# Optimization experiments

Measured on AMD Instinct MI355X. Metric: run time of the kernel, lower is better.

The kernel has to match this reference:

```python
import jax, jax.numpy as jnp
import numpy as np

N, R, E, DIN, DOUT, B = 40000, 16, 50000, 256, 256, 4


def setup_inputs() -> dict:
    key = jax.random.key(0)
    ks = jax.random.split(key, 7)
    xav = (2.0 / (DIN + DOUT)) ** 0.5  # xavier-ish scale
    x = jax.random.normal(ks[0], (N, DIN), jnp.float32)
    bases = jax.random.normal(ks[1], (B, DIN, DOUT), jnp.float32) * xav
    coeff = jax.random.normal(ks[2], (R, B), jnp.float32) * 0.5
    loop_weight = jax.random.normal(ks[3], (DIN, DOUT), jnp.float32) * xav
    h_bias = jnp.zeros((DOUT,), jnp.float32)
    edge_src = jax.random.randint(ks[4], (R, E), 0, N, dtype=jnp.int64)
    edge_dst = jax.random.randint(ks[5], (R, E), 0, N, dtype=jnp.int64)
    return {"x": x, "bases": bases, "coeff": coeff, "loop_weight": loop_weight,
            "h_bias": h_bias, "edge_src": edge_src, "edge_dst": edge_dst}


def reference(x, bases, coeff, loop_weight, h_bias, edge_src, edge_dst):
    # Basis decomposition: per-relation weight W_r = sum_b coeff[r,b] * bases[b]
    W = jnp.einsum('rb,bio->rio', coeff, bases)  # [R, DIN, DOUT]
    n = x.shape[0]

    def body(acc, rel):
        W_r, src, dst = rel
        # transform all nodes once, gather at edge sources
        m = (x @ W_r)[src]                                   # [E, DOUT]
        agg = jax.ops.segment_sum(m, dst, num_segments=n)    # [N, DOUT]
        deg = jax.ops.segment_sum(jnp.ones(src.shape, jnp.float32), dst,
                                  num_segments=n)            # in-degree per rel
        # norm='right': divide by dst in-degree (clamped to 1)
        return acc + agg / jnp.clip(deg, 1.0)[:, None], None

    h0 = jnp.zeros((n, loop_weight.shape[1]), x.dtype)
    h, _ = jax.lax.scan(body, h0, (W, edge_src, edge_dst))   # sum over relations
    h = h + x @ loop_weight + h_bias                         # self-loop + bias
    return jax.nn.relu(h)
```

## Files before the change

kernel.cpp:

```cpp
#include <hip/hip_runtime.h>

#define NN   40000
#define RR   16
#define EE   50000
#define DD   256
#define NB   4
#define KTOT (NB*DD + DD)
#define BM   64
#define BN   128
#define BK   32

#define SCAN_BLK  40
#define SCAN_ELEM 1024

typedef __bf16 bf16x8 __attribute__((ext_vector_type(8)));
typedef float  f32x4  __attribute__((ext_vector_type(4)));
typedef float  f32x2  __attribute__((ext_vector_type(2)));
typedef unsigned short ushort_t;

__device__ inline unsigned short f2bf(float f) {
    unsigned int b = __builtin_bit_cast(unsigned int, f);
    b += 0x7FFFu + ((b >> 16) & 1u);
    return (unsigned short)(b >> 16);
}


__global__ __launch_bounds__(256) void k_cast(const float* __restrict__ x,
                                              const float* __restrict__ bases,
                                              const float* __restrict__ lw,
                                              ushort_t* __restrict__ xb,
                                              ushort_t* __restrict__ Bt) {
    int t = blockIdx.x * blockDim.x + threadIdx.x;
    const int NX = NN * DD / 4;
    if (t < NX) {
        float4 f = *(const float4*)(x + (size_t)t * 4);
        ushort4 o;
        o.x = f2bf(f.x); o.y = f2bf(f.y); o.z = f2bf(f.z); o.w = f2bf(f.w);
        *(ushort4*)(xb + (size_t)t * 4) = o;
    } else {
        int u = t - NX;
        if (u < DD * KTOT) {
            int o = u / KTOT, k = u - o * KTOT;
            float f = (k < NB * DD) ? bases[(size_t)k * DD + o]
                                    : lw[(size_t)(k - NB * DD) * DD + o];
            Bt[u] = f2bf(f);
        }
    }
}

__global__ __launch_bounds__(256) void k_deg(const int* __restrict__ edst,
                                             int* __restrict__ deg) {
    int e = blockIdx.x * blockDim.x + threadIdx.x;
    if (e >= RR * EE) return;
    int r = e / EE;
    atomicAdd(&deg[r * NN + edst[e]], 1);
}

__global__ __launch_bounds__(256) void k_scanA(const int* __restrict__ deg,
                                               int* __restrict__ offsets,
                                               int* __restrict__ bsum) {
    __shared__ int part[256];
    int t = threadIdx.x, b = blockIdx.x;
    int g = b * SCAN_ELEM + t * 4;
    int4 h = {0, 0, 0, 0};
    if (g < NN) {
#pragma unroll
        for (int r = 0; r < RR; r++) {
            int4 d = *(const int4*)(deg + (size_t)r * NN + g);
            h.x += d.x; h.y += d.y; h.z += d.z; h.w += d.w;
        }
    }
    int s = h.x + h.y + h.z + h.w;
    part[t] = s;
    __syncthreads();
    for (int off = 1; off < 256; off <<= 1) {
        int v = (t >= off) ? part[t - off] : 0;
        __syncthreads();
        part[t] += v;
        __syncthreads();
    }
    int ex = part[t] - s;
    if (g < NN) {
        int4 o;
        o.x = ex;
        o.y = ex + h.x;
        o.z = ex + h.x + h.y;
        o.w = ex + h.x + h.y + h.z;
        *(int4*)(offsets + g) = o;
    }
    if (t == 255) bsum[b] = part[255];
}

__global__ __launch_bounds__(256) void k_scanB(const int* __restrict__ bsum,
                                               int* __restrict__ offsets,
                                               int* __restrict__ cursor) {
    __shared__ int sbase, stot;
    int t = threadIdx.x, b = blockIdx.x;
    if (t == 0) {
        int acc = 0, base = 0;
        for (int i = 0; i < SCAN_BLK; i++) {
            if (i == b) base = acc;
            acc += bsum[i];
        }
        sbase = base;
        stot = acc;
    }
    __syncthreads();
    int base = sbase;
    int g = b * SCAN_ELEM + t * 4;
    if (g < NN) {
        int4 o = *(const int4*)(offsets + g);
        o.x += base; o.y += base; o.z += base; o.w += base;
        *(int4*)(offsets + g) = o;
        *(int4*)(cursor + g) = o;
    }
    if (b == SCAN_BLK - 1 && t == 0) offsets[NN] = stot;
}

__global__ __launch_bounds__(256) void k_escatter(const int* __restrict__ esrc,
                                                  const int* __restrict__ edst,
                                                  int* __restrict__ cursor,
                                                  unsigned int* __restrict__ recs) {
    int e = blockIdx.x * blockDim.x + threadIdx.x;
    if (e >= RR * EE) return;
    int r = e / EE;
    int d = edst[e];
    int pos = atomicAdd(&cursor[d], 1);
    recs[pos] = (unsigned int)esrc[e] | ((unsigned int)r << 16);
}

__global__ __launch_bounds__(256) void k_gather(const ushort_t* __restrict__ xb,
                                                const float* __restrict__ coeff,
                                                const int* __restrict__ deg,
                                                const int* __restrict__ offsets,
                                                const unsigned int* __restrict__ recs,
                                                ushort_t* __restrict__ vb) {
    __shared__ float wtab[4][64];
    int lane = threadIdx.x & 63;
    int wv   = threadIdx.x >> 6;
    int n    = __builtin_amdgcn_readfirstlane(blockIdx.x * 4 + wv);

    {
        int r  = lane >> 2;
        int dg = deg[r * NN + n];
        float inv = 1.0f / (float)(dg > 0 ? dg : 1);
        wtab[wv][lane] = coeff[lane] * inv;
    }

    int beg = offsets[n], end = offsets[n + 1];
    f32x2 a[4][2];
#pragma unroll
    for (int b = 0; b < 4; b++) { a[b][0] = (f32x2){0,0}; a[b][1] = (f32x2){0,0}; }

    const float* wrow = &wtab[wv][0];
    const ushort_t* xl = xb + lane * 4;

    auto acc_edge = [&](uint2 u, float4 w) {
        f32x2 lo, hi;
        lo.x = __builtin_bit_cast(float, u.x << 16);
        lo.y = __builtin_bit_cast(float, u.x & 0xFFFF0000u);
        hi.x = __builtin_bit_cast(float, u.y << 16);
        hi.y = __builtin_bit_cast(float, u.y & 0xFFFF0000u);
        a[0][0] = lo * (f32x2){w.x, w.x} + a[0][0];
        a[0][1] = hi * (f32x2){w.x, w.x} + a[0][1];
        a[1][0] = lo * (f32x2){w.y, w.y} + a[1][0];
        a[1][1] = hi * (f32x2){w.y, w.y} + a[1][1];
        a[2][0] = lo * (f32x2){w.z, w.z} + a[2][0];
        a[2][1] = hi * (f32x2){w.z, w.z} + a[2][1];
        a[3][0] = lo * (f32x2){w.w, w.w} + a[3][0];
        a[3][1] = hi * (f32x2){w.w, w.w} + a[3][1];
    };

    int ei = beg;
    for (; ei + 4 <= end; ei += 4) {
        unsigned int r0 = recs[ei + 0];
        unsigned int r1 = recs[ei + 1];
        unsigned int r2 = recs[ei + 2];
        unsigned int r3 = recs[ei + 3];
        uint2 u0 = *(const uint2*)(xl + (size_t)(r0 & 0xFFFFu) * DD);
        uint2 u1 = *(const uint2*)(xl + (size_t)(r1 & 0xFFFFu) * DD);
        uint2 u2 = *(const uint2*)(xl + (size_t)(r2 & 0xFFFFu) * DD);
        uint2 u3 = *(const uint2*)(xl + (size_t)(r3 & 0xFFFFu) * DD);
        float4 w0 = *(const float4*)&wrow[(r0 >> 16) * 4];
        float4 w1 = *(const float4*)&wrow[(r1 >> 16) * 4];
        float4 w2 = *(const float4*)&wrow[(r2 >> 16) * 4];
        float4 w3 = *(const float4*)&wrow[(r3 >> 16) * 4];
        acc_edge(u0, w0);
        acc_edge(u1, w1);
        acc_edge(u2, w2);
        acc_edge(u3, w3);
    }
    for (; ei < end; ei++) {
        unsigned int r0 = recs[ei];
        uint2 u0 = *(const uint2*)(xl + (size_t)(r0 & 0xFFFFu) * DD);
        float4 w0 = *(const float4*)&wrow[(r0 >> 16) * 4];
        acc_edge(u0, w0);
    }

    ushort_t* vr = vb + (size_t)n * (NB * DD) + lane * 4;
#pragma unroll
    for (int b = 0; b < 4; b++) {
        ushort4 o;
        o.x = f2bf(a[b][0].x); o.y = f2bf(a[b][0].y);
        o.z = f2bf(a[b][1].x); o.w = f2bf(a[b][1].y);
        *(ushort4*)(vr + b * DD) = o;
    }
}

__global__ __launch_bounds__(256) void k_gemm(const ushort_t* __restrict__ vb,
                                              const ushort_t* __restrict__ xb,
                                              const ushort_t* __restrict__ Bt,
                                              const float* __restrict__ bias,
                                              float* __restrict__ out) {
    __shared__ ushort_t As[BM * BK];
    __shared__ ushort_t Bs[BN * BK];
    int tid  = threadIdx.x;
    int lane = tid & 63;
    int w    = tid >> 6;
    int wr   = w >> 1, wc = w & 1;
    int rowbase = blockIdx.x * BM;
    int nbase   = blockIdx.y * BN;
    int ml = lane & 15, q = lane >> 4;

    f32x4 acc[2][4];
#pragma unroll
    for (int i = 0; i < 2; i++)
#pragma unroll
        for (int j = 0; j < 4; j++) acc[i][j] = (f32x4){0,0,0,0};

    int srow = tid >> 2, sc = tid & 3;
    const ushort_t* bp0 = Bt + (size_t)(nbase + srow) * KTOT + sc * 8;
    const ushort_t* bp1 = Bt + (size_t)(nbase + 64 + srow) * KTOT + sc * 8;

    uint4 pa, pb0, pb1;

    auto g_load = [&](int kb) {
        const ushort_t* ap = (kb < NB * DD)
            ? vb + (size_t)(rowbase + srow) * (NB * DD) + kb + sc * 8
            : xb + (size_t)(rowbase + srow) * DD + (kb - NB * DD) + sc * 8;
        pa  = *(const uint4*)ap;
        pb0 = *(const uint4*)(bp0 + kb);
        pb1 = *(const uint4*)(bp1 + kb);
    };

    int soff = srow * BK + ((sc ^ (srow & 3)) * 8);

    g_load(0);
    for (int kb = 0; kb < KTOT; kb += BK) {
        __syncthreads();
        *(uint4*)&As[soff] = pa;
        *(uint4*)&Bs[soff] = pb0;
        *(uint4*)&Bs[64 * BK + soff] = pb1;
        __syncthreads();
        if (kb + BK < KTOT) g_load(kb + BK);

        bf16x8 af[2], bf[4];
#pragma unroll
        for (int i = 0; i < 2; i++) {
            int m = wr * 32 + i * 16 + ml;
            af[i] = *(const bf16x8*)&As[m * BK + ((q ^ (m & 3)) * 8)];
        }
#pragma unroll
        for (int j = 0; j < 4; j++) {
            int n = wc * 64 + j * 16 + ml;
            bf[j] = *(const bf16x8*)&Bs[n * BK + ((q ^ (n & 3)) * 8)];
        }
#pragma unroll
        for (int i = 0; i < 2; i++)
#pragma unroll
            for (int j = 0; j < 4; j++)
                acc[i][j] = __builtin_amdgcn_mfma_f32_16x16x32_bf16(af[i], bf[j], acc[i][j], 0, 0, 0);
    }

#pragma unroll
    for (int i = 0; i < 2; i++) {
#pragma unroll
        for (int r = 0; r < 4; r++) {
            int ng = rowbase + wr * 32 + i * 16 + q * 4 + r;
#pragma unroll
            for (int j = 0; j < 4; j++) {
                int o = nbase + wc * 64 + j * 16 + ml;
                float vv = acc[i][j][r] + bias[o];
                out[(size_t)ng * DD + o] = fmaxf(vv, 0.0f);
            }
        }
    }
}

extern "C" void kernel_launch(void* const* d_in, const int* in_sizes, int n_in,
                              void* d_out, int out_size, void* d_ws, size_t ws_size,
                              hipStream_t stream) {
    const float* x     = (const float*)d_in[0];
    const float* bases = (const float*)d_in[1];
    const float* coeff = (const float*)d_in[2];
    const float* lw    = (const float*)d_in[3];
    const float* bias  = (const float*)d_in[4];
    const int*   esrc  = (const int*)d_in[5];
    const int*   edst  = (const int*)d_in[6];
    float* out = (float*)d_out;

    char* ws = (char*)d_ws;
    ushort_t*     vb      = (ushort_t*)(ws);
    ushort_t*     xb      = (ushort_t*)(ws + 81920000);
    ushort_t*     Bt      = (ushort_t*)(ws + 102400000);
    int*          deg     = (int*)(ws + 103055360);
    int*          offsets = (int*)(ws + 105775360);
    int*          cursor  = (int*)(ws + 105935376);
    unsigned int* recs    = (unsigned int*)(ws + 106095376);
    int*          bsum    = (int*)(ws + 109295376);

    hipMemsetAsync(deg, 0, (size_t)RR * NN * sizeof(int), stream);

    int ne = RR * EE;
    int ncast = NN * DD / 4 + DD * KTOT;
    k_cast<<<(ncast + 255) / 256, 256, 0, stream>>>(x, bases, lw, xb, Bt);
    k_deg<<<(ne + 255) / 256, 256, 0, stream>>>(edst, deg);
    k_scanA<<<SCAN_BLK, 256, 0, stream>>>(deg, offsets, bsum);
    k_scanB<<<SCAN_BLK, 256, 0, stream>>>(bsum, offsets, cursor);
    k_escatter<<<(ne + 255) / 256, 256, 0, stream>>>(esrc, edst, cursor, recs);
    k_gather<<<NN / 4, 256, 0, stream>>>(xb, coeff, deg, offsets, recs, vb);
    dim3 ggrid(NN / BM, DD / BN);
    k_gemm<<<ggrid, 256, 0, stream>>>(vb, xb, Bt, bias, out);
}
```

Baseline: 308.9 us.

## Double-buffer GEMM shared tiles, fix LDS swizzle, merge cast and degree kernels

```diff
diff --git a/kernel.cpp b/kernel.cpp
--- a/kernel.cpp
+++ b/kernel.cpp
@@ -9,6 +9,7 @@
 #define BM   64
 #define BN   128
 #define BK   32
+#define NITER (KTOT/BK)
 
 #define SCAN_BLK  40
 #define SCAN_ELEM 1024
@@ -25,35 +26,41 @@
 }
 
 
-__global__ __launch_bounds__(256) void k_cast(const float* __restrict__ x,
+#define CAST_BLKS ((NN * DD / 4 + DD * KTOT + 255) / 256)
+#define DEG_BLKS  ((RR * EE + 255) / 256)
+
+__global__ __launch_bounds__(256) void k_prep(const float* __restrict__ x,
                                               const float* __restrict__ bases,
                                               const float* __restrict__ lw,
+                                              const int* __restrict__ edst,
                                               ushort_t* __restrict__ xb,
-                                              ushort_t* __restrict__ Bt) {
-    int t = blockIdx.x * blockDim.x + threadIdx.x;
-    const int NX = NN * DD / 4;
-    if (t < NX) {
-        float4 f = *(const float4*)(x + (size_t)t * 4);
-        ushort4 o;
-        o.x = f2bf(f.x); o.y = f2bf(f.y); o.z = f2bf(f.z); o.w = f2bf(f.w);
-        *(ushort4*)(xb + (size_t)t * 4) = o;
+                                              ushort_t* __restrict__ Bt,
+                                              int* __restrict__ deg) {
+    int b = blockIdx.x;
+    if (b < CAST_BLKS) {
+        int t = b * 256 + threadIdx.x;
+        const int NX = NN * DD / 4;
+        if (t < NX) {
+            float4 f = *(const float4*)(x + (size_t)t * 4);
+            ushort4 o;
+            o.x = f2bf(f.x); o.y = f2bf(f.y); o.z = f2bf(f.z); o.w = f2bf(f.w);
+            *(ushort4*)(xb + (size_t)t * 4) = o;
+        } else {
+            int u = t - NX;
+            if (u < DD * KTOT) {
+                int o = u / KTOT, k = u - o * KTOT;
+                float f = (k < NB * DD) ? bases[(size_t)k * DD + o]
+                                        : lw[(size_t)(k - NB * DD) * DD + o];
+                Bt[u] = f2bf(f);
+            }
+        }
     } else {
-        int u = t - NX;
-        if (u < DD * KTOT) {
-            int o = u / KTOT, k = u - o * KTOT;
-            float f = (k < NB * DD) ? bases[(size_t)k * DD + o]
-                                    : lw[(size_t)(k - NB * DD) * DD + o];
-            Bt[u] = f2bf(f);
-        }
-    }
-}
-
-__global__ __launch_bounds__(256) void k_deg(const int* __restrict__ edst,
-                                             int* __restrict__ deg) {
-    int e = blockIdx.x * blockDim.x + threadIdx.x;
-    if (e >= RR * EE) return;
-    int r = e / EE;
-    atomicAdd(&deg[r * NN + edst[e]], 1);
+        int e = (b - CAST_BLKS) * 256 + threadIdx.x;
+        if (e < RR * EE) {
+            int r = e / EE;
+            atomicAdd(&deg[r * NN + edst[e]], 1);
+        }
+    }
 }
 
 __global__ __launch_bounds__(256) void k_scanA(const int* __restrict__ deg,
@@ -212,8 +219,8 @@
                                               const ushort_t* __restrict__ Bt,
                                               const float* __restrict__ bias,
                                               float* __restrict__ out) {
-    __shared__ ushort_t As[BM * BK];
-    __shared__ ushort_t Bs[BN * BK];
+    __shared__ ushort_t As[2][BM * BK];
+    __shared__ ushort_t Bs[2][BN * BK];
     int tid  = threadIdx.x;
     int lane = tid & 63;
     int w    = tid >> 6;
@@ -232,39 +239,47 @@
     const ushort_t* bp0 = Bt + (size_t)(nbase + srow) * KTOT + sc * 8;
     const ushort_t* bp1 = Bt + (size_t)(nbase + 64 + srow) * KTOT + sc * 8;
 
-    uint4 pa, pb0, pb1;
-
-    auto g_load = [&](int kb) {
+    uint4 pa[2], pb0[2], pb1[2];
+
+    auto g_load = [&](int kb, int s) {
         const ushort_t* ap = (kb < NB * DD)
             ? vb + (size_t)(rowbase + srow) * (NB * DD) + kb + sc * 8
             : xb + (size_t)(rowbase + srow) * DD + (kb - NB * DD) + sc * 8;
-        pa  = *(const uint4*)ap;
-        pb0 = *(const uint4*)(bp0 + kb);
-        pb1 = *(const uint4*)(bp1 + kb);
+        pa[s]  = *(const uint4*)ap;
+        pb0[s] = *(const uint4*)(bp0 + kb);
+        pb1[s] = *(const uint4*)(bp1 + kb);
     };
 
-    int soff = srow * BK + ((sc ^ (srow & 3)) * 8);
-
-    g_load(0);
-    for (int kb = 0; kb < KTOT; kb += BK) {
+    int soff = srow * BK + ((sc ^ ((srow >> 2) & 3)) * 8);
+
+    int aoff[2], boff[4];
+#pragma unroll
+    for (int i = 0; i < 2; i++) {
+        int m = wr * 32 + i * 16 + ml;
+        aoff[i] = m * BK + ((q ^ ((m >> 2) & 3)) * 8);
+    }
+#pragma unroll
+    for (int j = 0; j < 4; j++) {
+        int n = wc * 64 + j * 16 + ml;
+        boff[j] = n * BK + ((q ^ ((n >> 2) & 3)) * 8);
+    }
+
+    g_load(0, 0);
+    g_load(BK, 1);
+#pragma unroll 2
+    for (int it = 0; it < NITER; it++) {
+        int s = it & 1;
+        *(uint4*)&As[s][soff] = pa[s];
+        *(uint4*)&Bs[s][soff] = pb0[s];
+        *(uint4*)&Bs[s][64 * BK + soff] = pb1[s];
+        if (it + 2 < NITER) g_load((it + 2) * BK, s);
         __syncthreads();
-        *(uint4*)&As[soff] = pa;
-        *(uint4*)&Bs[soff] = pb0;
-        *(uint4*)&Bs[64 * BK + soff] = pb1;
-        __syncthreads();
-        if (kb + BK < KTOT) g_load(kb + BK);
 
         bf16x8 af[2], bf[4];
 #pragma unroll
-        for (int i = 0; i < 2; i++) {
-            int m = wr * 32 + i * 16 + ml;
-            af[i] = *(const bf16x8*)&As[m * BK + ((q ^ (m & 3)) * 8)];
-        }
-#pragma unroll
-        for (int j = 0; j < 4; j++) {
-            int n = wc * 64 + j * 16 + ml;
-            bf[j] = *(const bf16x8*)&Bs[n * BK + ((q ^ (n & 3)) * 8)];
-        }
+        for (int i = 0; i < 2; i++) af[i] = *(const bf16x8*)&As[s][aoff[i]];
+#pragma unroll
+        for (int j = 0; j < 4; j++) bf[j] = *(const bf16x8*)&Bs[s][boff[j]];
 #pragma unroll
         for (int i = 0; i < 2; i++)
 #pragma unroll
@@ -312,9 +327,7 @@
     hipMemsetAsync(deg, 0, (size_t)RR * NN * sizeof(int), stream);
 
     int ne = RR * EE;
-    int ncast = NN * DD / 4 + DD * KTOT;
-    k_cast<<<(ncast + 255) / 256, 256, 0, stream>>>(x, bases, lw, xb, Bt);
-    k_deg<<<(ne + 255) / 256, 256, 0, stream>>>(edst, deg);
+    k_prep<<<CAST_BLKS + DEG_BLKS, 256, 0, stream>>>(x, bases, lw, edst, xb, Bt, deg);
     k_scanA<<<SCAN_BLK, 256, 0, stream>>>(deg, offsets, bsum);
     k_scanB<<<SCAN_BLK, 256, 0, stream>>>(bsum, offsets, cursor);
     k_escatter<<<(ne + 255) / 256, 256, 0, stream>>>(esrc, edst, cursor, recs);
```

Result: slower. 439.5 us (+42.3%).
